# Performance work log

Hardware: AMD Instinct MI355X
Metric: run time of the kernel (lower is better)

## Reference

```python
import jax, jax.numpy as jnp
import numpy as np

ZETA = 1.1
GAMMA = -0.1

B, F, D = 1024, 32, 128


def setup_inputs() -> dict:
    key = jax.random.key(0)
    k1, k2 = jax.random.split(key)
    feature = jax.random.normal(k1, (B, F, D), dtype=jnp.float32)
    # nn.Parameter init: normal(mean=0, std=0.001)
    matrix = jax.random.normal(k2, (F, F, D, D), dtype=jnp.float32) * 0.001
    return {"feature": feature, "matrix": matrix}


def reference(feature, matrix):
    # feature: [B, F, D]; matrix (logAlpha of hard-concrete gate): [F, F, D, D]
    nF = matrix.shape[0]
    # strict upper-triangular pair mask over (i, j)
    mask = jnp.triu(jnp.ones((nF, nF), dtype=feature.dtype), k=1)
    # deterministic (eval-mode) hard-concrete gate: stretch + clamp
    s = jax.nn.sigmoid(matrix)
    z = jnp.clip(s * (ZETA - GAMMA) + GAMMA, 0.0, 1.0)
    l0_out = mask[:, :, None, None] * z  # [F, F, D, D]
    # out[b,i,j] = f_i^T Z_ij f_j  == sum_{d,e} f[b,i,d] * Z[i,j,d,e] * f[b,j,e]
    # (faithful to: (f[:, :, None, :, None] @ f[:, None, :, None, :]) * Z, summed over (d, e))
    out = jnp.einsum('bid,ijde,bje->bij', feature, l0_out, feature)
    return out
```

## Files before the change

### kernel.cpp

```cpp
#include <hip/hip_runtime.h>

#define B_SZ 1024
#define F_SZ 32
#define D_SZ 128
#define FD   4096
#define NPAIR 496

typedef __bf16 bf16x8 __attribute__((ext_vector_type(8)));
typedef float floatx4 __attribute__((ext_vector_type(4)));
typedef unsigned short u16x8 __attribute__((ext_vector_type(8)));

__device__ __forceinline__ unsigned short f2bf(float f) {
  unsigned u = __float_as_uint(f);
  u += 0x7fffu + ((u >> 16) & 1u);
  return (unsigned short)(u >> 16);
}

__global__ __launch_bounds__(256, 2)
void interaction_fused_kernel(const float* __restrict__ feat,
                              const float* __restrict__ mat,
                              float* __restrict__ out) {
  __shared__ unsigned short sZT[128 * 128];
  __shared__ unsigned short sS[128 * 128];

  const int t    = threadIdx.x;
  const int w    = t >> 6;
  const int lane = t & 63;
  const int l15  = lane & 15;
  const int quad = lane >> 4;

  const int bid   = blockIdx.x;
  const int pid   = bid >> 2;
  const int split = bid & 3;
  int p = pid, i = 0;
  while (p >= F_SZ - 1 - i) { p -= F_SZ - 1 - i; ++i; }
  const int j = i + 1 + p;

  if (bid < B_SZ) {
    const int ii = t >> 3, s = t & 7;
    float* ob = out + (size_t)bid * (F_SZ * F_SZ) + ii * F_SZ;
    #pragma unroll
    for (int c = 0; c < 4; ++c) {
      int jj = s * 4 + c;
      if (jj <= ii) ob[jj] = 0.f;
    }
  }

  {
    const float* zp = mat + (((size_t)i * F_SZ + j) * (size_t)(D_SZ * D_SZ));
    #pragma unroll
    for (int it = 0; it < 16; ++it) {
      int idx4 = it * 256 + t;
      int d = idx4 >> 5, e4 = (idx4 & 31) * 4;
      const float4 v = *(const float4*)(zp + (size_t)d * D_SZ + e4);
      float zs[4] = {v.x, v.y, v.z, v.w};
      ushort4 h;
      unsigned short* hp = &h.x;
      #pragma unroll
      for (int c = 0; c < 4; ++c) {
        float s = 1.0f / (1.0f + __expf(-zs[c]));
        hp[c] = f2bf(fminf(1.0f, fmaxf(0.0f, fmaf(s, 1.2f, -0.1f))));
      }
      *(ushort4*)&sS[d * D_SZ + e4] = h;
    }
  }
  __syncthreads();

  {
    #pragma unroll
    for (int it = 0; it < 8; ++it) {
      int u = it * 256 + t;
      int e = u & 127, g = u >> 7;
      u16x8 pk;
      #pragma unroll
      for (int r = 0; r < 8; ++r) pk[r] = sS[(g * 8 + r) * D_SZ + e];
      *(u16x8*)&sZT[e * D_SZ + (g ^ (e & 7)) * 8] = pk;
    }
  }
  __syncthreads();

  #pragma unroll 1
  for (int pass = 0; pass < 2; ++pass) {
    const int rbase = split * 256 + pass * 128;

    #pragma unroll
    for (int it = 0; it < 16; ++it) {
      int idx4 = it * 256 + t;
      int r = idx4 >> 5, c4 = idx4 & 31;
      const float4 v = *(const float4*)(feat + (size_t)(rbase + r) * FD +
                                        i * D_SZ + c4 * 4);
      ushort4 h;
      h.x = f2bf(v.x); h.y = f2bf(v.y); h.z = f2bf(v.z); h.w = f2bf(v.w);
      const int grp = c4 >> 1, half8 = (c4 & 1) * 8;
      *(ushort4*)((char*)sS + r * 256 + ((grp ^ (r & 7)) * 16 + half8)) = h;
    }
    __syncthreads();

    floatx4 acc[2][8];
    #pragma unroll
    for (int mf = 0; mf < 2; ++mf)
      #pragma unroll
      for (int nf = 0; nf < 8; ++nf)
        acc[mf][nf] = (floatx4){0.f, 0.f, 0.f, 0.f};

    const int row0 = w * 32 + l15;
    #pragma unroll
    for (int k0 = 0; k0 < 4; ++k0) {
      const int kb = k0 * 64 + quad * 16;
      bf16x8 a0 = *(const bf16x8*)((const char*)sS + row0 * 256 +
                                   (kb ^ ((row0 & 7) << 4)));
      bf16x8 a1 = *(const bf16x8*)((const char*)sS + (row0 + 16) * 256 +
                                   (kb ^ ((row0 & 7) << 4)));
      #pragma unroll
      for (int nf = 0; nf < 8; ++nf) {
        const int e = nf * 16 + l15;
        bf16x8 bf = *(const bf16x8*)((const char*)sZT + e * 256 +
                                     (kb ^ ((e & 7) << 4)));
        acc[0][nf] = __builtin_amdgcn_mfma_f32_16x16x32_bf16(a0, bf, acc[0][nf], 0, 0, 0);
        acc[1][nf] = __builtin_amdgcn_mfma_f32_16x16x32_bf16(a1, bf, acc[1][nf], 0, 0, 0);
      }
    }

    #pragma unroll
    for (int mf = 0; mf < 2; ++mf) {
      float pl[4] = {0.f, 0.f, 0.f, 0.f};
      const int rg = rbase + w * 32 + mf * 16 + quad * 4;
      #pragma unroll
      for (int nf = 0; nf < 8; ++nf) {
        const int col = nf * 16 + l15;
        const float* fj = feat + (size_t)rg * FD + j * D_SZ + col;
        floatx4 c = acc[mf][nf];
        pl[0] += c[0] * fj[0];
        pl[1] += c[1] * fj[FD];
        pl[2] += c[2] * fj[2 * FD];
        pl[3] += c[3] * fj[3 * FD];
      }
      #pragma unroll
      for (int off = 1; off < 16; off <<= 1) {
        pl[0] += __shfl_xor(pl[0], off, 64);
        pl[1] += __shfl_xor(pl[1], off, 64);
        pl[2] += __shfl_xor(pl[2], off, 64);
        pl[3] += __shfl_xor(pl[3], off, 64);
      }
      if (l15 == 0) {
        size_t ob = (size_t)rg * (F_SZ * F_SZ) + (size_t)i * F_SZ + j;
        out[ob]                   = pl[0];
        out[ob + 1 * F_SZ * F_SZ] = pl[1];
        out[ob + 2 * F_SZ * F_SZ] = pl[2];
        out[ob + 3 * F_SZ * F_SZ] = pl[3];
      }
    }
    __syncthreads();
  }
}

extern "C" void kernel_launch(void* const* d_in, const int* in_sizes, int n_in,
                              void* d_out, int out_size, void* d_ws, size_t ws_size,
                              hipStream_t stream) {
  const float* feat = (const float*)d_in[0];
  const float* mat  = (const float*)d_in[1];
  float* out = (float*)d_out;

  interaction_fused_kernel<<<dim3(NPAIR * 4), dim3(256), 0, stream>>>(feat, mat, out);
}
```

Measured before the change: 152.7 us.

## One block per pair over full batch, A fragments loaded straight into registers

Each (i,j) pair now gets a single block that loops over all 1024 batch rows, so the Z gate matrix is computed, converted and transposed once per pair rather than four times. Feature rows for operand A are read from global memory directly into MFMA register fragments and converted to bf16, which removes the shared-memory staging and both per-pass barriers. The trade-off is a grid of only 496 blocks, which lowers parallelism and leaves less latency hiding on the MI355X's many CUs. The global A loads are also less coalesced, since each lane reads 32-byte chunks scattered across rows.

New measurement: 146.4 us. 4.1% less time.

```diff
diff --git a/kernel.cpp b/kernel.cpp
--- a/kernel.cpp
+++ b/kernel.cpp
@@ -16,6 +16,13 @@
   return (unsigned short)(u >> 16);
 }
 
+__device__ __forceinline__ bf16x8 cvt8(float4 v0, float4 v1) {
+  union { u16x8 u; bf16x8 b; } r;
+  r.u[0] = f2bf(v0.x); r.u[1] = f2bf(v0.y); r.u[2] = f2bf(v0.z); r.u[3] = f2bf(v0.w);
+  r.u[4] = f2bf(v1.x); r.u[5] = f2bf(v1.y); r.u[6] = f2bf(v1.z); r.u[7] = f2bf(v1.w);
+  return r.b;
+}
+
 __global__ __launch_bounds__(256, 2)
 void interaction_fused_kernel(const float* __restrict__ feat,
                               const float* __restrict__ mat,
@@ -29,16 +36,14 @@
   const int l15  = lane & 15;
   const int quad = lane >> 4;
 
-  const int bid   = blockIdx.x;
-  const int pid   = bid >> 2;
-  const int split = bid & 3;
-  int p = pid, i = 0;
+  const int bid = blockIdx.x;
+  int p = bid, i = 0;
   while (p >= F_SZ - 1 - i) { p -= F_SZ - 1 - i; ++i; }
   const int j = i + 1 + p;
 
-  if (bid < B_SZ) {
+  for (int bb = bid; bb < B_SZ; bb += NPAIR) {
     const int ii = t >> 3, s = t & 7;
-    float* ob = out + (size_t)bid * (F_SZ * F_SZ) + ii * F_SZ;
+    float* ob = out + (size_t)bb * (F_SZ * F_SZ) + ii * F_SZ;
     #pragma unroll
     for (int c = 0; c < 4; ++c) {
       int jj = s * 4 + c;
@@ -80,21 +85,21 @@
   __syncthreads();
 
   #pragma unroll 1
-  for (int pass = 0; pass < 2; ++pass) {
-    const int rbase = split * 256 + pass * 128;
+  for (int pass = 0; pass < 8; ++pass) {
+    const int rbase = pass * 128 + w * 32;
 
-    #pragma unroll
-    for (int it = 0; it < 16; ++it) {
-      int idx4 = it * 256 + t;
-      int r = idx4 >> 5, c4 = idx4 & 31;
-      const float4 v = *(const float4*)(feat + (size_t)(rbase + r) * FD +
-                                        i * D_SZ + c4 * 4);
-      ushort4 h;
-      h.x = f2bf(v.x); h.y = f2bf(v.y); h.z = f2bf(v.z); h.w = f2bf(v.w);
-      const int grp = c4 >> 1, half8 = (c4 & 1) * 8;
-      *(ushort4*)((char*)sS + r * 256 + ((grp ^ (r & 7)) * 16 + half8)) = h;
+    bf16x8 a0[4], a1[4];
+    {
+      const float* ap0 = feat + (size_t)(rbase + l15) * FD + i * D_SZ + quad * 8;
+      const float* ap1 = ap0 + (size_t)16 * FD;
+      #pragma unroll
+      for (int k0 = 0; k0 < 4; ++k0) {
+        a0[k0] = cvt8(*(const float4*)(ap0 + k0 * 32),
+                      *(const float4*)(ap0 + k0 * 32 + 4));
+        a1[k0] = cvt8(*(const float4*)(ap1 + k0 * 32),
+                      *(const float4*)(ap1 + k0 * 32 + 4));
+      }
     }
-    __syncthreads();
 
     floatx4 acc[2][8];
     #pragma unroll
@@ -103,28 +108,23 @@
       for (int nf = 0; nf < 8; ++nf)
         acc[mf][nf] = (floatx4){0.f, 0.f, 0.f, 0.f};
 
-    const int row0 = w * 32 + l15;
     #pragma unroll
     for (int k0 = 0; k0 < 4; ++k0) {
       const int kb = k0 * 64 + quad * 16;
-      bf16x8 a0 = *(const bf16x8*)((const char*)sS + row0 * 256 +
-                                   (kb ^ ((row0 & 7) << 4)));
-      bf16x8 a1 = *(const bf16x8*)((const char*)sS + (row0 + 16) * 256 +
-                                   (kb ^ ((row0 & 7) << 4)));
       #pragma unroll
       for (int nf = 0; nf < 8; ++nf) {
         const int e = nf * 16 + l15;
         bf16x8 bf = *(const bf16x8*)((const char*)sZT + e * 256 +
                                      (kb ^ ((e & 7) << 4)));
-        acc[0][nf] = __builtin_amdgcn_mfma_f32_16x16x32_bf16(a0, bf, acc[0][nf], 0, 0, 0);
-        acc[1][nf] = __builtin_amdgcn_mfma_f32_16x16x32_bf16(a1, bf, acc[1][nf], 0, 0, 0);
+        acc[0][nf] = __builtin_amdgcn_mfma_f32_16x16x32_bf16(a0[k0], bf, acc[0][nf], 0, 0, 0);
+        acc[1][nf] = __builtin_amdgcn_mfma_f32_16x16x32_bf16(a1[k0], bf, acc[1][nf], 0, 0, 0);
       }
     }
 
     #pragma unroll
     for (int mf = 0; mf < 2; ++mf) {
       float pl[4] = {0.f, 0.f, 0.f, 0.f};
-      const int rg = rbase + w * 32 + mf * 16 + quad * 4;
+      const int rg = rbase + mf * 16 + quad * 4;
       #pragma unroll
       for (int nf = 0; nf < 8; ++nf) {
         const int col = nf * 16 + l15;
@@ -150,7 +150,6 @@
         out[ob + 3 * F_SZ * F_SZ] = pl[3];
       }
     }
-    __syncthreads();
   }
 }
 
@@ -161,5 +160,5 @@
   const float* mat  = (const float*)d_in[1];
   float* out = (float*)d_out;
 
-  interaction_fused_kernel<<<dim3(NPAIR * 4), dim3(256), 0, stream>>>(feat, mat, out);
+  interaction_fused_kernel<<<dim3(NPAIR), dim3(256), 0, stream>>>(feat, mat, out);
 }
```
